# Performance work log

Measured on AMD Instinct MI355X. Metric: run time of the kernel, lower is better.

The kernel has to match this reference:

```python
import jax, jax.numpy as jnp
import numpy as np

B, H, V, T = 32, 1024, 32000, 64

def setup_inputs() -> dict:
    key = jax.random.key(0)
    ks = jax.random.split(key, 8)
    s = 1.0 / np.sqrt(H)
    return {
        "hidden_state": jax.random.normal(ks[0], (1, B, H), jnp.float32),
        "cell_state": jax.random.normal(ks[1], (1, B, H), jnp.float32),
        "W_ih": jax.random.normal(ks[2], (4 * H, H), jnp.float32) * s,
        "W_hh": jax.random.normal(ks[3], (4 * H, H), jnp.float32) * s,
        "b_ih": jax.random.normal(ks[4], (4 * H,), jnp.float32) * s,
        "b_hh": jax.random.normal(ks[5], (4 * H,), jnp.float32) * s,
        "W_out": jax.random.normal(ks[6], (V, H), jnp.float32) * s,
        "b_out": jax.random.normal(ks[7], (V,), jnp.float32) * s,
        "output_len": T,
    }

def reference(hidden_state, cell_state, W_ih, W_hh, b_ih, b_hh, W_out, b_out, output_len):
    h0 = hidden_state[0]  # [B, H]
    c0 = cell_state[0]    # [B, H]
    Hd = h0.shape[-1]
    # Decoder input is all-zeros every step (as in the torch code), so the
    # input-to-hidden contribution reduces to the constant bias b_ih.
    x_gates = jnp.zeros_like(h0) @ W_ih.T + b_ih  # [B, 4H] (keeps W_ih in the graph)

    def step(carry, _):
        h, c = carry
        gates = x_gates + h @ W_hh.T + b_hh  # [B, 4H], torch gate order i,f,g,o
        i, f, g, o = jnp.split(gates, 4, axis=-1)
        c = jax.nn.sigmoid(f) * c + jax.nn.sigmoid(i) * jnp.tanh(g)
        h = jax.nn.sigmoid(o) * jnp.tanh(c)
        logp = jax.nn.log_softmax(h @ W_out.T + b_out, axis=-1)  # [B, V]
        return (h, c), logp

    _, ys = jax.lax.scan(step, (h0, c0), None, length=output_len)  # [T, B, V]
    return jnp.transpose(ys, (1, 0, 2))  # [B, T, V]
```

## Files before the change

kernel.cpp:

```cpp
#include <hip/hip_runtime.h>
#include <hip/hip_bf16.h>
#include <math.h>

#define HD 1024
#define BD 32
#define TD 64
#define VD 32000
#define NWG 128
#define GW  512
#define NTM 16
#define NTN 250

typedef __attribute__((ext_vector_type(8))) short bf16x8;
typedef __attribute__((ext_vector_type(4))) float f32x4;

__device__ __forceinline__ short f2bf(float x) {
    __hip_bfloat16 h = __float2bfloat16(x);
    union { __hip_bfloat16 h; short s; } u; u.h = h; return u.s;
}
__device__ __forceinline__ float fsigmoid(float x) {
    return 1.f / (1.f + __expf(-x));
}
__device__ __forceinline__ float ftanh(float x) {
    return 1.f - 2.f / (__expf(2.f * x) + 1.f);
}


__global__ __launch_bounds__(256) void init_kernel(
    const float* __restrict__ Whh_f, const float* __restrict__ bih,
    const float* __restrict__ bhh,  const float* __restrict__ Wout_f,
    const float* __restrict__ h0,
    short* __restrict__ Whh_b, short* __restrict__ Wout_b,
    float* __restrict__ bias,  short* __restrict__ hb, int* __restrict__ ctr)
{
    long i0 = (long)blockIdx.x * blockDim.x + threadIdx.x;
    long stride = (long)gridDim.x * blockDim.x;
    for (long i = i0; i < 21 * TD; i += stride) ctr[i] = 0;
    for (long i = i0; i < (long)VD * HD / 4; i += stride) {
        float4 x = ((const float4*)Wout_f)[i];
        short4 y; y.x = f2bf(x.x); y.y = f2bf(x.y); y.z = f2bf(x.z); y.w = f2bf(x.w);
        ((short4*)Wout_b)[i] = y;
    }
    for (long i = i0; i < (long)4 * HD * HD / 4; i += stride) {
        float4 x = ((const float4*)Whh_f)[i];
        short4 y; y.x = f2bf(x.x); y.y = f2bf(x.y); y.z = f2bf(x.z); y.w = f2bf(x.w);
        ((short4*)Whh_b)[i] = y;
    }
    for (long i = i0; i < 4 * HD; i += stride) bias[i] = bih[i] + bhh[i];
    for (long i = i0; i < BD * HD; i += stride) {
        int b = (int)(i >> 10), j = (int)(i & 1023);
        int kq = j >> 8, ks = (j >> 5) & 7, hi = (j >> 3) & 3, e = j & 7;
        int u = ((kq * 8 + ks) * 2 + (b >> 4)) * 64 + hi * 16 + (b & 15);
        hb[u * 8 + e] = f2bf(h0[i]);
    }
}

__global__ __launch_bounds__(256, 2) void fused_lstm_gemm(
    const short* __restrict__ Whh_b,
    const float* __restrict__ bias,
    const float* __restrict__ c0,
    short* __restrict__ hb,
    short* __restrict__ Hmat,
    const short* __restrict__ Bw,
    const float* __restrict__ bout,
    float* __restrict__ C,
    int* __restrict__ ctrS,
    int* __restrict__ ctrQ,
    int* __restrict__ queue)
{
    __shared__ alignas(16) char shmem[32768];
    __shared__ int tau_sh;
    const int tid = threadIdx.x;

    if (blockIdx.x < NWG) {
        float (*gl)[32][36] = (float (*)[32][36])shmem;
        const int w = blockIdx.x;
        const int kq = tid >> 6;
        const int l = tid & 63;
        const int lo = l & 15, hi = l >> 4;
        const int j0 = w * 8;
        const int kbase = kq * 256 + hi * 8;

        const short* wB0 = Whh_b + (long)((lo >> 3) * HD + j0 + (lo & 7)) * HD + kbase;
        const short* wB1 = Whh_b + (long)(((16 + lo) >> 3) * HD + j0 + ((16 + lo) & 7)) * HD + kbase;
        bf16x8 wb0[8], wb1[8];
        #pragma unroll
        for (int ks = 0; ks < 8; ks++) {
            wb0[ks] = *(const bf16x8*)(wB0 + ks * 32);
            wb1[ks] = *(const bf16x8*)(wB1 + ks * 32);
        }

        const int cb = tid >> 3, cjl = tid & 7;
        float creg = c0[cb * HD + j0 + cjl];
        const float bi  = bias[j0 + cjl];
        const float bf_ = bias[HD + j0 + cjl];
        const float bg  = bias[2 * HD + j0 + cjl];
        const float bo_ = bias[3 * HD + j0 + cjl];

        const int kq0 = w >> 5, ks0 = (w >> 2) & 7, hi0 = w & 3;
        const int sg = (w >> 3) & 3;
        const int ust = ((kq0 * 8 + ks0) * 2 + (cb >> 4)) * 64 + hi0 * 16 + (cb & 15);

        for (int t = 0; t < TD; ++t) {
            if (t > 0) {
                const int* cq = &ctrQ[kq * TD + (t - 1)];
                while (__hip_atomic_load(cq, __ATOMIC_RELAXED, __HIP_MEMORY_SCOPE_AGENT) < 4)
                    __builtin_amdgcn_s_sleep(1);
            }
            const short* hrb = hb + (size_t)(t & 1) * (BD * HD);

            bf16x8 a0[8], a1[8];
            #pragma unroll
            for (int ks = 0; ks < 8; ks++) {
                const short* p0 = hrb + ((size_t)(((kq * 8 + ks) * 2 + 0) * 64 + l)) * 8;
                const short* p1 = hrb + ((size_t)(((kq * 8 + ks) * 2 + 1) * 64 + l)) * 8;
                asm volatile("global_load_dwordx4 %0, %1, off sc1"
                             : "=v"(a0[ks]) : "v"(p0) : "memory");
                asm volatile("global_load_dwordx4 %0, %1, off sc1"
                             : "=v"(a1[ks]) : "v"(p1) : "memory");
            }
            asm volatile("s_waitcnt vmcnt(0)" ::: "memory");
            __builtin_amdgcn_sched_barrier(0);

            f32x4 acc[2][2] = {};
            #pragma unroll
            for (int ks = 0; ks < 8; ks++) {
                acc[0][0] = __builtin_amdgcn_mfma_f32_16x16x32_bf16(a0[ks], wb0[ks], acc[0][0], 0, 0, 0);
                acc[0][1] = __builtin_amdgcn_mfma_f32_16x16x32_bf16(a0[ks], wb1[ks], acc[0][1], 0, 0, 0);
                acc[1][0] = __builtin_amdgcn_mfma_f32_16x16x32_bf16(a1[ks], wb0[ks], acc[1][0], 0, 0, 0);
                acc[1][1] = __builtin_amdgcn_mfma_f32_16x16x32_bf16(a1[ks], wb1[ks], acc[1][1], 0, 0, 0);
            }
            #pragma unroll
            for (int mf = 0; mf < 2; mf++)
                #pragma unroll
                for (int nf = 0; nf < 2; nf++)
                    #pragma unroll
                    for (int r = 0; r < 4; r++)
                        gl[kq][mf * 16 + hi * 4 + r][nf * 16 + lo] = acc[mf][nf][r];
            __syncthreads();

            float xi = gl[0][cb][cjl]      + gl[1][cb][cjl]      + gl[2][cb][cjl]      + gl[3][cb][cjl]      + bi;
            float xf = gl[0][cb][8 + cjl]  + gl[1][cb][8 + cjl]  + gl[2][cb][8 + cjl]  + gl[3][cb][8 + cjl]  + bf_;
            float xg = gl[0][cb][16 + cjl] + gl[1][cb][16 + cjl] + gl[2][cb][16 + cjl] + gl[3][cb][16 + cjl] + bg;
            float xo = gl[0][cb][24 + cjl] + gl[1][cb][24 + cjl] + gl[2][cb][24 + cjl] + gl[3][cb][24 + cjl] + bo_;
            float cn = fsigmoid(xf) * creg + fsigmoid(xi) * ftanh(xg);
            float hn = fsigmoid(xo) * ftanh(cn);
            creg = cn;
            short hv = f2bf(hn);
            {
                unsigned int hval = (unsigned short)hv;
                short* hm  = Hmat + ((size_t)t * BD + cb) * HD + j0 + cjl;
                short* hwb = hb + (size_t)((t + 1) & 1) * (BD * HD) + (size_t)ust * 8 + cjl;
                asm volatile("global_store_short %0, %1, off sc1" :: "v"(hm),  "v"(hval) : "memory");
                asm volatile("global_store_short %0, %1, off sc1" :: "v"(hwb), "v"(hval) : "memory");
            }
            asm volatile("s_waitcnt vmcnt(0)" ::: "memory");
            __syncthreads();

            if (tid == 0) {
                int old = __hip_atomic_fetch_add(&ctrS[(kq0 * 4 + sg) * TD + t], 1,
                                                 __ATOMIC_RELAXED, __HIP_MEMORY_SCOPE_AGENT);
                if (old == 7)
                    __hip_atomic_fetch_add(&ctrQ[kq0 * TD + t], 1,
                                           __ATOMIC_RELAXED, __HIP_MEMORY_SCOPE_AGENT);
            }
        }
    } else {
        short* lds = (short*)shmem;
        const int lane = tid & 63, wv = tid >> 6;
        const int lo = lane & 15, hi = lane >> 4;
        const int wm = wv >> 1, wn = wv & 1;

        const int u0 = tid, u1 = tid + 256;
        const int r0 = (u0 >> 3) * 2 + (u0 & 1);
        const int r1 = (u1 >> 3) * 2 + (u1 & 1);
        const int kc0 = (((u0 & 7) - (r0 & 7)) & 7) >> 1;
        const int kc1 = (((u1 & 7) - (r1 & 7)) & 7) >> 1;

        int unitA[4], unitB[4];
        #pragma unroll
        for (int mf = 0; mf < 4; mf++) {
            int row = wm * 64 + mf * 16 + lo;
            unitA[mf] = (row >> 1) * 8 + ((2 * hi + (row & 7)) & 7);
        }
        #pragma unroll
        for (int nf = 0; nf < 4; nf++) {
            int row = wn * 64 + nf * 16 + lo;
            unitB[nf] = 512 + (row >> 1) * 8 + ((2 * hi + (row & 7)) & 7);
        }

        for (;;) {
            if (tid == 0)
                tau_sh = __hip_atomic_fetch_add(queue, 1, __ATOMIC_RELAXED, __HIP_MEMORY_SCOPE_AGENT);
            __syncthreads();
            int tau = tau_sh;
            if (tau >= NTM * NTN) break;
            int m = tau / NTN, n = tau - m * NTN;

            if (tid == 0) {
                int tr = m * 4 + 3;
                #pragma unroll
                for (int q = 0; q < 4; q++)
                    while (__hip_atomic_load(&ctrQ[q * TD + tr], __ATOMIC_RELAXED,
                                             __HIP_MEMORY_SCOPE_AGENT) < 4)
                        __builtin_amdgcn_s_sleep(8);
            }
            __syncthreads();

            const short* pA0 = Hmat + ((long)m * 128 + r0) * HD + kc0 * 8;
            const short* pA1 = Hmat + ((long)m * 128 + r1) * HD + kc1 * 8;
            const short* pB0 = Bw + ((long)n * 128 + r0) * HD + kc0 * 8;
            const short* pB1 = Bw + ((long)n * 128 + r1) * HD + kc1 * 8;

#define GSTAGE(koff, bb) do { \
    __builtin_amdgcn_global_load_lds((const __attribute__((address_space(1))) short*)(pA0 + (koff)), \
        (__attribute__((address_space(3))) short*)&lds[((bb) + u0) * 8], 16, 0, 0); \
    __builtin_amdgcn_global_load_lds((const __attribute__((address_space(1))) short*)(pA1 + (koff)), \
        (__attribute__((address_space(3))) short*)&lds[((bb) + u1) * 8], 16, 0, 0); \
    __builtin_amdgcn_global_load_lds((const __attribute__((address_space(1))) short*)(pB0 + (koff)), \
        (__attribute__((address_space(3))) short*)&lds[((bb) + 512 + u0) * 8], 16, 0, 0); \
    __builtin_amdgcn_global_load_lds((const __attribute__((address_space(1))) short*)(pB1 + (koff)), \
        (__attribute__((address_space(3))) short*)&lds[((bb) + 512 + u1) * 8], 16, 0, 0); \
} while (0)

            f32x4 acc[4][4] = {};
            GSTAGE(0, 0);
            GSTAGE(32, 1024);
            asm volatile("s_waitcnt vmcnt(4)\n\ts_barrier" ::: "memory");

            for (int kt = 0; kt < 32; ++kt) {
                const int bb = (kt & 1) * 1024;
                bf16x8 a[4], b[4];
                #pragma unroll
                for (int mf = 0; mf < 4; mf++) a[mf] = *(const bf16x8*)&lds[(bb + unitA[mf]) * 8];
                #pragma unroll
                for (int nf = 0; nf < 4; nf++) b[nf] = *(const bf16x8*)&lds[(bb + unitB[nf]) * 8];
                __builtin_amdgcn_s_setprio(1);
                #pragma unroll
                for (int mf = 0; mf < 4; mf++)
                    #pragma unroll
                    for (int nf = 0; nf < 4; nf++)
                        acc[mf][nf] = __builtin_amdgcn_mfma_f32_16x16x32_bf16(a[mf], b[nf], acc[mf][nf], 0, 0, 0);
                __builtin_amdgcn_s_setprio(0);
                __builtin_amdgcn_s_barrier();
                if (kt + 2 < 32) {
                    GSTAGE((kt + 2) * 32, bb);
                    asm volatile("s_waitcnt vmcnt(4)" ::: "memory");
                } else {
                    asm volatile("s_waitcnt vmcnt(0)" ::: "memory");
                }
                __builtin_amdgcn_s_barrier();
            }
#undef GSTAGE

            float bo[4];
            #pragma unroll
            for (int nf = 0; nf < 4; nf++) bo[nf] = bout[n * 128 + wn * 64 + nf * 16 + lo];
            #pragma unroll
            for (int mf = 0; mf < 4; mf++)
                #pragma unroll
                for (int r = 0; r < 4; r++) {
                    int trow = m * 128 + wm * 64 + mf * 16 + hi * 4 + r;
                    int bt = trow & 31, tt = trow >> 5;
                    float* cp = C + ((long)bt * TD + tt) * VD + n * 128 + wn * 64 + lo;
                    #pragma unroll
                    for (int nf = 0; nf < 4; nf++)
                        cp[nf * 16] = acc[mf][nf][r] + bo[nf];
                }
            __syncthreads();
        }
    }
}

__global__ __launch_bounds__(256) void logsoftmax_inplace(float* __restrict__ C)
{
    const long row = blockIdx.x;
    float* p = C + row * (long)VD;
    const int tid = threadIdx.x;
    float m = -3.4e38f, s = 0.f;
    for (int i = tid; i < VD / 4; i += 256) {
        float4 x = ((const float4*)p)[i];
        float mx = fmaxf(fmaxf(x.x, x.y), fmaxf(x.z, x.w));
        if (mx > m) { s *= __expf(m - mx); m = mx; }
        s += __expf(x.x - m) + __expf(x.y - m) + __expf(x.z - m) + __expf(x.w - m);
    }
    #pragma unroll
    for (int off = 32; off > 0; off >>= 1) {
        float m2 = __shfl_xor(m, off, 64);
        float s2 = __shfl_xor(s, off, 64);
        float mn = fmaxf(m, m2);
        s = s * __expf(m - mn) + s2 * __expf(m2 - mn);
        m = mn;
    }
    __shared__ float sm[4], ss[4];
    if ((tid & 63) == 0) { sm[tid >> 6] = m; ss[tid >> 6] = s; }
    __syncthreads();
    float M = fmaxf(fmaxf(sm[0], sm[1]), fmaxf(sm[2], sm[3]));
    float S = ss[0] * __expf(sm[0] - M) + ss[1] * __expf(sm[1] - M) +
              ss[2] * __expf(sm[2] - M) + ss[3] * __expf(sm[3] - M);
    float lse = M + logf(S);
    for (int i = tid; i < VD / 4; i += 256) {
        float4 x = ((float4*)p)[i];
        x.x -= lse; x.y -= lse; x.z -= lse; x.w -= lse;
        ((float4*)p)[i] = x;
    }
}

extern "C" void kernel_launch(void* const* d_in, const int* in_sizes, int n_in,
                              void* d_out, int out_size, void* d_ws, size_t ws_size,
                              hipStream_t stream)
{
    const float* h0   = (const float*)d_in[0];
    const float* c0   = (const float*)d_in[1];
    const float* Whh  = (const float*)d_in[3];
    const float* bih  = (const float*)d_in[4];
    const float* bhh  = (const float*)d_in[5];
    const float* Wout = (const float*)d_in[6];
    const float* bout = (const float*)d_in[7];

    char* ws = (char*)d_ws;
    short* Wout_b = (short*)ws;  ws += (size_t)VD * HD * 2;
    short* Whh_b  = (short*)ws;  ws += (size_t)4 * HD * HD * 2;
    short* Hmat   = (short*)ws;  ws += (size_t)BD * TD * HD * 2;
    short* hb     = (short*)ws;  ws += (size_t)2 * BD * HD * 2;
    float* bias   = (float*)ws;  ws += (size_t)4 * HD * 4;
    int*   ctr    = (int*)ws;    ws += 21 * TD * sizeof(int);
    float* C      = (float*)d_out;

    int* ctrS  = ctr;
    int* ctrQ  = ctr + 16 * TD;
    int* queue = ctr + 20 * TD;

    init_kernel<<<2048, 256, 0, stream>>>(Whh, bih, bhh, Wout, h0,
                                          Whh_b, Wout_b, bias, hb, ctr);
    fused_lstm_gemm<<<NWG + GW, 256, 0, stream>>>(Whh_b, bias, c0, hb, Hmat,
                                                  Wout_b, bout, C, ctrS, ctrQ, queue);
    logsoftmax_inplace<<<2048, 256, 0, stream>>>(C);
}
```

Before: 502.1 us.

## Fuse softmax row-sum into output GEMM epilogue and enlarge M tile to 256

New measurement: 482.3 us. 3.9% less time.

```diff
diff --git a/kernel.cpp b/kernel.cpp
--- a/kernel.cpp
+++ b/kernel.cpp
@@ -8,8 +8,9 @@
 #define VD 32000
 #define NWG 128
 #define GW  512
-#define NTM 16
+#define NPH 8
 #define NTN 250
+#define NTT (NPH * NTN)
 
 typedef __attribute__((ext_vector_type(8))) short bf16x8;
 typedef __attribute__((ext_vector_type(4))) float f32x4;
@@ -31,11 +32,13 @@
     const float* __restrict__ bhh,  const float* __restrict__ Wout_f,
     const float* __restrict__ h0,
     short* __restrict__ Whh_b, short* __restrict__ Wout_b,
-    float* __restrict__ bias,  short* __restrict__ hb, int* __restrict__ ctr)
+    float* __restrict__ bias,  short* __restrict__ hb, int* __restrict__ ctr,
+    float* __restrict__ rowsum)
 {
     long i0 = (long)blockIdx.x * blockDim.x + threadIdx.x;
     long stride = (long)gridDim.x * blockDim.x;
     for (long i = i0; i < 21 * TD; i += stride) ctr[i] = 0;
+    for (long i = i0; i < BD * TD; i += stride) rowsum[i] = 0.f;
     for (long i = i0; i < (long)VD * HD / 4; i += stride) {
         float4 x = ((const float4*)Wout_f)[i];
         short4 y; y.x = f2bf(x.x); y.y = f2bf(x.y); y.z = f2bf(x.z); y.w = f2bf(x.w);
@@ -64,15 +67,17 @@
     const short* __restrict__ Bw,
     const float* __restrict__ bout,
     float* __restrict__ C,
+    float* __restrict__ rowsum,
     int* __restrict__ ctrS,
     int* __restrict__ ctrQ,
     int* __restrict__ queue)
 {
-    __shared__ alignas(16) char shmem[32768];
+    __shared__ alignas(16) char shmem[50176];
     __shared__ int tau_sh;
     const int tid = threadIdx.x;
 
     if (blockIdx.x < NWG) {
+        __builtin_amdgcn_s_setprio(2);
         float (*gl)[32][36] = (float (*)[32][36])shmem;
         const int w = blockIdx.x;
         const int kq = tid >> 6;
@@ -167,26 +172,35 @@
         }
     } else {
         short* lds = (short*)shmem;
+        float* rowsum_sh = (float*)(shmem + 49152);
         const int lane = tid & 63, wv = tid >> 6;
         const int lo = lane & 15, hi = lane >> 4;
         const int wm = wv >> 1, wn = wv & 1;
 
-        const int u0 = tid, u1 = tid + 256;
-        const int r0 = (u0 >> 3) * 2 + (u0 & 1);
-        const int r1 = (u1 >> 3) * 2 + (u1 & 1);
-        const int kc0 = (((u0 & 7) - (r0 & 7)) & 7) >> 1;
-        const int kc1 = (((u1 & 7) - (r1 & 7)) & 7) >> 1;
-
-        int unitA[4], unitB[4];
-        #pragma unroll
-        for (int mf = 0; mf < 4; mf++) {
-            int row = wm * 64 + mf * 16 + lo;
+        int rA[4], kA[4], rB[2], kB[2];
+        #pragma unroll
+        for (int i = 0; i < 4; i++) {
+            int u = tid + i * 256;
+            rA[i] = (u >> 3) * 2 + (u & 1);
+            kA[i] = (((u & 7) - (rA[i] & 7)) & 7) >> 1;
+        }
+        #pragma unroll
+        for (int i = 0; i < 2; i++) {
+            int u = tid + i * 256;
+            rB[i] = (u >> 3) * 2 + (u & 1);
+            kB[i] = (((u & 7) - (rB[i] & 7)) & 7) >> 1;
+        }
+
+        int unitA[8], unitB[4];
+        #pragma unroll
+        for (int mf = 0; mf < 8; mf++) {
+            int row = wm * 128 + mf * 16 + lo;
             unitA[mf] = (row >> 1) * 8 + ((2 * hi + (row & 7)) & 7);
         }
         #pragma unroll
         for (int nf = 0; nf < 4; nf++) {
-            int row = wn * 64 + nf * 16 + lo;
-            unitB[nf] = 512 + (row >> 1) * 8 + ((2 * hi + (row & 7)) & 7);
+            int brow = wn * 64 + nf * 16 + lo;
+            unitB[nf] = 1024 + (brow >> 1) * 8 + ((2 * hi + (brow & 7)) & 7);
         }
 
         for (;;) {
@@ -194,11 +208,11 @@
                 tau_sh = __hip_atomic_fetch_add(queue, 1, __ATOMIC_RELAXED, __HIP_MEMORY_SCOPE_AGENT);
             __syncthreads();
             int tau = tau_sh;
-            if (tau >= NTM * NTN) break;
-            int m = tau / NTN, n = tau - m * NTN;
+            if (tau >= NTT) break;
+            int p = tau / NTN, n = tau - p * NTN;
 
             if (tid == 0) {
-                int tr = m * 4 + 3;
+                int tr = p * 8 + 7;
                 #pragma unroll
                 for (int q = 0; q < 4; q++)
                     while (__hip_atomic_load(&ctrQ[q * TD + tr], __ATOMIC_RELAXED,
@@ -207,37 +221,43 @@
             }
             __syncthreads();
 
-            const short* pA0 = Hmat + ((long)m * 128 + r0) * HD + kc0 * 8;
-            const short* pA1 = Hmat + ((long)m * 128 + r1) * HD + kc1 * 8;
-            const short* pB0 = Bw + ((long)n * 128 + r0) * HD + kc0 * 8;
-            const short* pB1 = Bw + ((long)n * 128 + r1) * HD + kc1 * 8;
+            const short* pA0 = Hmat + ((long)p * 256 + rA[0]) * HD + kA[0] * 8;
+            const short* pA1 = Hmat + ((long)p * 256 + rA[1]) * HD + kA[1] * 8;
+            const short* pA2 = Hmat + ((long)p * 256 + rA[2]) * HD + kA[2] * 8;
+            const short* pA3 = Hmat + ((long)p * 256 + rA[3]) * HD + kA[3] * 8;
+            const short* pB0 = Bw + ((long)n * 128 + rB[0]) * HD + kB[0] * 8;
+            const short* pB1 = Bw + ((long)n * 128 + rB[1]) * HD + kB[1] * 8;
 
 #define GSTAGE(koff, bb) do { \
     __builtin_amdgcn_global_load_lds((const __attribute__((address_space(1))) short*)(pA0 + (koff)), \
-        (__attribute__((address_space(3))) short*)&lds[((bb) + u0) * 8], 16, 0, 0); \
+        (__attribute__((address_space(3))) short*)&lds[((bb) + tid) * 8], 16, 0, 0); \
     __builtin_amdgcn_global_load_lds((const __attribute__((address_space(1))) short*)(pA1 + (koff)), \
-        (__attribute__((address_space(3))) short*)&lds[((bb) + u1) * 8], 16, 0, 0); \
+        (__attribute__((address_space(3))) short*)&lds[((bb) + tid + 256) * 8], 16, 0, 0); \
+    __builtin_amdgcn_global_load_lds((const __attribute__((address_space(1))) short*)(pA2 + (koff)), \
+        (__attribute__((address_space(3))) short*)&lds[((bb) + tid + 512) * 8], 16, 0, 0); \
+    __builtin_amdgcn_global_load_lds((const __attribute__((address_space(1))) short*)(pA3 + (koff)), \
+        (__attribute__((address_space(3))) short*)&lds[((bb) + tid + 768) * 8], 16, 0, 0); \
     __builtin_amdgcn_global_load_lds((const __attribute__((address_space(1))) short*)(pB0 + (koff)), \
-        (__attribute__((address_space(3))) short*)&lds[((bb) + 512 + u0) * 8], 16, 0, 0); \
+        (__attribute__((address_space(3))) short*)&lds[((bb) + 1024 + tid) * 8], 16, 0, 0); \
     __builtin_amdgcn_global_load_lds((const __attribute__((address_space(1))) short*)(pB1 + (koff)), \
-        (__attribute__((address_space(3))) short*)&lds[((bb) + 512 + u1) * 8], 16, 0, 0); \
+        (__attribute__((address_space(3))) short*)&lds[((bb) + 1024 + tid + 256) * 8], 16, 0, 0); \
 } while (0)
 
-            f32x4 acc[4][4] = {};
+            f32x4 acc[8][4] = {};
             GSTAGE(0, 0);
-            GSTAGE(32, 1024);
-            asm volatile("s_waitcnt vmcnt(4)\n\ts_barrier" ::: "memory");
+            GSTAGE(32, 1536);
+            asm volatile("s_waitcnt vmcnt(6)\n\ts_barrier" ::: "memory");
 
             for (int kt = 0; kt < 32; ++kt) {
-                const int bb = (kt & 1) * 1024;
-                bf16x8 a[4], b[4];
-                #pragma unroll
-                for (int mf = 0; mf < 4; mf++) a[mf] = *(const bf16x8*)&lds[(bb + unitA[mf]) * 8];
+                const int bb = (kt & 1) * 1536;
+                bf16x8 a[8], b[4];
+                #pragma unroll
+                for (int mf = 0; mf < 8; mf++) a[mf] = *(const bf16x8*)&lds[(bb + unitA[mf]) * 8];
                 #pragma unroll
                 for (int nf = 0; nf < 4; nf++) b[nf] = *(const bf16x8*)&lds[(bb + unitB[nf]) * 8];
                 __builtin_amdgcn_s_setprio(1);
                 #pragma unroll
-                for (int mf = 0; mf < 4; mf++)
+                for (int mf = 0; mf < 8; mf++)
                     #pragma unroll
                     for (int nf = 0; nf < 4; nf++)
                         acc[mf][nf] = __builtin_amdgcn_mfma_f32_16x16x32_bf16(a[mf], b[nf], acc[mf][nf], 0, 0, 0);
@@ -245,7 +265,7 @@
                 __builtin_amdgcn_s_barrier();
                 if (kt + 2 < 32) {
                     GSTAGE((kt + 2) * 32, bb);
-                    asm volatile("s_waitcnt vmcnt(4)" ::: "memory");
+                    asm volatile("s_waitcnt vmcnt(6)" ::: "memory");
                 } else {
                     asm volatile("s_waitcnt vmcnt(0)" ::: "memory");
                 }
@@ -253,54 +273,54 @@
             }
 #undef GSTAGE
 
+            rowsum_sh[tid] = 0.f;
+            __syncthreads();
             float bo[4];
             #pragma unroll
             for (int nf = 0; nf < 4; nf++) bo[nf] = bout[n * 128 + wn * 64 + nf * 16 + lo];
             #pragma unroll
-            for (int mf = 0; mf < 4; mf++)
+            for (int mf = 0; mf < 8; mf++)
                 #pragma unroll
                 for (int r = 0; r < 4; r++) {
-                    int trow = m * 128 + wm * 64 + mf * 16 + hi * 4 + r;
+                    int rloc = wm * 128 + mf * 16 + hi * 4 + r;
+                    int trow = p * 256 + rloc;
                     int bt = trow & 31, tt = trow >> 5;
                     float* cp = C + ((long)bt * TD + tt) * VD + n * 128 + wn * 64 + lo;
+                    float es = 0.f;
                     #pragma unroll
-                    for (int nf = 0; nf < 4; nf++)
-                        cp[nf * 16] = acc[mf][nf][r] + bo[nf];
+                    for (int nf = 0; nf < 4; nf++) {
+                        float v = acc[mf][nf][r] + bo[nf];
+                        cp[nf * 16] = v;
+                        es += __expf(v);
+                    }
+                    es += __shfl_xor(es, 1, 64);
+                    es += __shfl_xor(es, 2, 64);
+                    es += __shfl_xor(es, 4, 64);
+                    es += __shfl_xor(es, 8, 64);
+                    if (lo == 0) atomicAdd(&rowsum_sh[rloc], es);
                 }
             __syncthreads();
-        }
-    }
-}
-
-__global__ __launch_bounds__(256) void logsoftmax_inplace(float* __restrict__ C)
+            {
+                int trow = p * 256 + tid;
+                int bt = trow & 31, tt = trow >> 5;
+                float* rp = rowsum + bt * TD + tt;
+                float val = rowsum_sh[tid];
+                asm volatile("global_atomic_add_f32 %0, %1, off" :: "v"(rp), "v"(val) : "memory");
+            }
+            asm volatile("s_waitcnt vmcnt(0)" ::: "memory");
+            __syncthreads();
+        }
+    }
+}
+
+__global__ __launch_bounds__(256) void logsub(float* __restrict__ C,
+                                              const float* __restrict__ rowsum)
 {
     const long row = blockIdx.x;
     float* p = C + row * (long)VD;
-    const int tid = threadIdx.x;
-    float m = -3.4e38f, s = 0.f;
-    for (int i = tid; i < VD / 4; i += 256) {
+    const float lse = logf(rowsum[row]);
+    for (int i = threadIdx.x; i < VD / 4; i += 256) {
         float4 x = ((const float4*)p)[i];
-        float mx = fmaxf(fmaxf(x.x, x.y), fmaxf(x.z, x.w));
-        if (mx > m) { s *= __expf(m - mx); m = mx; }
-        s += __expf(x.x - m) + __expf(x.y - m) + __expf(x.z - m) + __expf(x.w - m);
-    }
-    #pragma unroll
-    for (int off = 32; off > 0; off >>= 1) {
-        float m2 = __shfl_xor(m, off, 64);
-        float s2 = __shfl_xor(s, off, 64);
-        float mn = fmaxf(m, m2);
-        s = s * __expf(m - mn) + s2 * __expf(m2 - mn);
-        m = mn;
-    }
-    __shared__ float sm[4], ss[4];
-    if ((tid & 63) == 0) { sm[tid >> 6] = m; ss[tid >> 6] = s; }
-    __syncthreads();
-    float M = fmaxf(fmaxf(sm[0], sm[1]), fmaxf(sm[2], sm[3]));
-    float S = ss[0] * __expf(sm[0] - M) + ss[1] * __expf(sm[1] - M) +
-              ss[2] * __expf(sm[2] - M) + ss[3] * __expf(sm[3] - M);
-    float lse = M + logf(S);
-    for (int i = tid; i < VD / 4; i += 256) {
-        float4 x = ((float4*)p)[i];
         x.x -= lse; x.y -= lse; x.z -= lse; x.w -= lse;
         ((float4*)p)[i] = x;
     }
@@ -325,6 +345,7 @@
     short* hb     = (short*)ws;  ws += (size_t)2 * BD * HD * 2;
     float* bias   = (float*)ws;  ws += (size_t)4 * HD * 4;
     int*   ctr    = (int*)ws;    ws += 21 * TD * sizeof(int);
+    float* rowsum = (float*)ws;  ws += (size_t)BD * TD * 4;
     float* C      = (float*)d_out;
 
     int* ctrS  = ctr;
@@ -332,8 +353,9 @@
     int* queue = ctr + 20 * TD;
 
     init_kernel<<<2048, 256, 0, stream>>>(Whh, bih, bhh, Wout, h0,
-                                          Whh_b, Wout_b, bias, hb, ctr);
+                                          Whh_b, Wout_b, bias, hb, ctr, rowsum);
     fused_lstm_gemm<<<NWG + GW, 256, 0, stream>>>(Whh_b, bias, c0, hb, Hmat,
-                                                  Wout_b, bout, C, ctrS, ctrQ, queue);
-    logsoftmax_inplace<<<2048, 256, 0, stream>>>(C);
-}
+                                                  Wout_b, bout, C, rowsum,
+                                                  ctrS, ctrQ, queue);
+    logsub<<<2048, 256, 0, stream>>>(C, rowsum);
+}
```

## Fuse softmax exp-sum into GEMM epilogue and use per-block step flags

Applied to the files above, without the earlier changes.

Result: slower. 608.4 us (+21.2%).

```diff
diff --git a/kernel.cpp b/kernel.cpp
--- a/kernel.cpp
+++ b/kernel.cpp
@@ -10,6 +10,7 @@
 #define GW  512
 #define NTM 16
 #define NTN 250
+#define NTT (NTM * NTN)
 
 typedef __attribute__((ext_vector_type(8))) short bf16x8;
 typedef __attribute__((ext_vector_type(4))) float f32x4;
@@ -31,11 +32,13 @@
     const float* __restrict__ bhh,  const float* __restrict__ Wout_f,
     const float* __restrict__ h0,
     short* __restrict__ Whh_b, short* __restrict__ Wout_b,
-    float* __restrict__ bias,  short* __restrict__ hb, int* __restrict__ ctr)
+    float* __restrict__ bias,  short* __restrict__ hb, int* __restrict__ ctr,
+    float* __restrict__ rowsum)
 {
     long i0 = (long)blockIdx.x * blockDim.x + threadIdx.x;
     long stride = (long)gridDim.x * blockDim.x;
-    for (long i = i0; i < 21 * TD; i += stride) ctr[i] = 0;
+    for (long i = i0; i < 256; i += stride) ctr[i] = 0;
+    for (long i = i0; i < BD * TD; i += stride) rowsum[i] = 0.f;
     for (long i = i0; i < (long)VD * HD / 4; i += stride) {
         float4 x = ((const float4*)Wout_f)[i];
         short4 y; y.x = f2bf(x.x); y.y = f2bf(x.y); y.z = f2bf(x.z); y.w = f2bf(x.w);
@@ -64,16 +67,18 @@
     const short* __restrict__ Bw,
     const float* __restrict__ bout,
     float* __restrict__ C,
-    int* __restrict__ ctrS,
-    int* __restrict__ ctrQ,
+    float* __restrict__ rowsum,
+    int* __restrict__ flags,
     int* __restrict__ queue)
 {
-    __shared__ alignas(16) char shmem[32768];
+    __shared__ alignas(16) short lds[2 * 1024 * 8];
+    __shared__ float rowsum_sh[128];
     __shared__ int tau_sh;
     const int tid = threadIdx.x;
 
     if (blockIdx.x < NWG) {
-        float (*gl)[32][36] = (float (*)[32][36])shmem;
+        __builtin_amdgcn_s_setprio(2);
+        float (*gl)[32][36] = (float (*)[32][36])lds;
         const int w = blockIdx.x;
         const int kq = tid >> 6;
         const int l = tid & 63;
@@ -98,14 +103,16 @@
         const float bo_ = bias[3 * HD + j0 + cjl];
 
         const int kq0 = w >> 5, ks0 = (w >> 2) & 7, hi0 = w & 3;
-        const int sg = (w >> 3) & 3;
         const int ust = ((kq0 * 8 + ks0) * 2 + (cb >> 4)) * 64 + hi0 * 16 + (cb & 15);
+        const int* fp = &flags[kq * 32 + (l & 31)];
 
         for (int t = 0; t < TD; ++t) {
             if (t > 0) {
-                const int* cq = &ctrQ[kq * TD + (t - 1)];
-                while (__hip_atomic_load(cq, __ATOMIC_RELAXED, __HIP_MEMORY_SCOPE_AGENT) < 4)
+                for (;;) {
+                    int f = __hip_atomic_load(fp, __ATOMIC_RELAXED, __HIP_MEMORY_SCOPE_AGENT);
+                    if (__all(f >= t)) break;
                     __builtin_amdgcn_s_sleep(1);
+                }
             }
             const short* hrb = hb + (size_t)(t & 1) * (BD * HD);
 
@@ -157,16 +164,10 @@
             asm volatile("s_waitcnt vmcnt(0)" ::: "memory");
             __syncthreads();
 
-            if (tid == 0) {
-                int old = __hip_atomic_fetch_add(&ctrS[(kq0 * 4 + sg) * TD + t], 1,
-                                                 __ATOMIC_RELAXED, __HIP_MEMORY_SCOPE_AGENT);
-                if (old == 7)
-                    __hip_atomic_fetch_add(&ctrQ[kq0 * TD + t], 1,
-                                           __ATOMIC_RELAXED, __HIP_MEMORY_SCOPE_AGENT);
-            }
+            if (tid == 0)
+                __hip_atomic_store(&flags[w], t + 1, __ATOMIC_RELAXED, __HIP_MEMORY_SCOPE_AGENT);
         }
     } else {
-        short* lds = (short*)shmem;
         const int lane = tid & 63, wv = tid >> 6;
         const int lo = lane & 15, hi = lane >> 4;
         const int wm = wv >> 1, wn = wv & 1;
@@ -194,18 +195,23 @@
                 tau_sh = __hip_atomic_fetch_add(queue, 1, __ATOMIC_RELAXED, __HIP_MEMORY_SCOPE_AGENT);
             __syncthreads();
             int tau = tau_sh;
-            if (tau >= NTM * NTN) break;
+            if (tau >= NTT) break;
             int m = tau / NTN, n = tau - m * NTN;
 
-            if (tid == 0) {
-                int tr = m * 4 + 3;
-                #pragma unroll
-                for (int q = 0; q < 4; q++)
-                    while (__hip_atomic_load(&ctrQ[q * TD + tr], __ATOMIC_RELAXED,
-                                             __HIP_MEMORY_SCOPE_AGENT) < 4)
-                        __builtin_amdgcn_s_sleep(8);
-            }
-            __syncthreads();
+            {
+                const int tgt = m * 4 + 4;
+                if (tid < 64) {
+                    const int* f0 = &flags[tid];
+                    const int* f1 = &flags[tid + 64];
+                    for (;;) {
+                        int a = __hip_atomic_load(f0, __ATOMIC_RELAXED, __HIP_MEMORY_SCOPE_AGENT);
+                        int b = __hip_atomic_load(f1, __ATOMIC_RELAXED, __HIP_MEMORY_SCOPE_AGENT);
+                        if (__all(a >= tgt && b >= tgt)) break;
+                        __builtin_amdgcn_s_sleep(16);
+                    }
+                }
+                __syncthreads();
+            }
 
             const short* pA0 = Hmat + ((long)m * 128 + r0) * HD + kc0 * 8;
             const short* pA1 = Hmat + ((long)m * 128 + r1) * HD + kc1 * 8;
@@ -253,6 +259,8 @@
             }
 #undef GSTAGE
 
+            if (tid < 128) rowsum_sh[tid] = 0.f;
+            __syncthreads();
             float bo[4];
             #pragma unroll
             for (int nf = 0; nf < 4; nf++) bo[nf] = bout[n * 128 + wn * 64 + nf * 16 + lo];
@@ -260,47 +268,45 @@
             for (int mf = 0; mf < 4; mf++)
                 #pragma unroll
                 for (int r = 0; r < 4; r++) {
-                    int trow = m * 128 + wm * 64 + mf * 16 + hi * 4 + r;
+                    int rloc = wm * 64 + mf * 16 + hi * 4 + r;
+                    int trow = m * 128 + rloc;
                     int bt = trow & 31, tt = trow >> 5;
                     float* cp = C + ((long)bt * TD + tt) * VD + n * 128 + wn * 64 + lo;
+                    float es = 0.f;
                     #pragma unroll
-                    for (int nf = 0; nf < 4; nf++)
-                        cp[nf * 16] = acc[mf][nf][r] + bo[nf];
+                    for (int nf = 0; nf < 4; nf++) {
+                        float v = acc[mf][nf][r] + bo[nf];
+                        cp[nf * 16] = v;
+                        es += __expf(v);
+                    }
+                    es += __shfl_xor(es, 1, 64);
+                    es += __shfl_xor(es, 2, 64);
+                    es += __shfl_xor(es, 4, 64);
+                    es += __shfl_xor(es, 8, 64);
+                    if (lo == 0) atomicAdd(&rowsum_sh[rloc], es);
                 }
             __syncthreads();
-        }
-    }
-}
-
-__global__ __launch_bounds__(256) void logsoftmax_inplace(float* __restrict__ C)
+            if (tid < 128) {
+                int trow = m * 128 + tid;
+                int bt = trow & 31, tt = trow >> 5;
+                float* rp = rowsum + bt * TD + tt;
+                float val = rowsum_sh[tid];
+                asm volatile("global_atomic_add_f32 %0, %1, off" :: "v"(rp), "v"(val) : "memory");
+            }
+            asm volatile("s_waitcnt vmcnt(0)" ::: "memory");
+            __syncthreads();
+        }
+    }
+}
+
+__global__ __launch_bounds__(256) void logsub(float* __restrict__ C,
+                                              const float* __restrict__ rowsum)
 {
     const long row = blockIdx.x;
     float* p = C + row * (long)VD;
-    const int tid = threadIdx.x;
-    float m = -3.4e38f, s = 0.f;
-    for (int i = tid; i < VD / 4; i += 256) {
+    const float lse = logf(rowsum[row]);
+    for (int i = threadIdx.x; i < VD / 4; i += 256) {
         float4 x = ((const float4*)p)[i];
-        float mx = fmaxf(fmaxf(x.x, x.y), fmaxf(x.z, x.w));
-        if (mx > m) { s *= __expf(m - mx); m = mx; }
-        s += __expf(x.x - m) + __expf(x.y - m) + __expf(x.z - m) + __expf(x.w - m);
-    }
-    #pragma unroll
-    for (int off = 32; off > 0; off >>= 1) {
-        float m2 = __shfl_xor(m, off, 64);
-        float s2 = __shfl_xor(s, off, 64);
-        float mn = fmaxf(m, m2);
-        s = s * __expf(m - mn) + s2 * __expf(m2 - mn);
-        m = mn;
-    }
-    __shared__ float sm[4], ss[4];
-    if ((tid & 63) == 0) { sm[tid >> 6] = m; ss[tid >> 6] = s; }
-    __syncthreads();
-    float M = fmaxf(fmaxf(sm[0], sm[1]), fmaxf(sm[2], sm[3]));
-    float S = ss[0] * __expf(sm[0] - M) + ss[1] * __expf(sm[1] - M) +
-              ss[2] * __expf(sm[2] - M) + ss[3] * __expf(sm[3] - M);
-    float lse = M + logf(S);
-    for (int i = tid; i < VD / 4; i += 256) {
-        float4 x = ((float4*)p)[i];
         x.x -= lse; x.y -= lse; x.z -= lse; x.w -= lse;
         ((float4*)p)[i] = x;
     }
@@ -324,16 +330,17 @@
     short* Hmat   = (short*)ws;  ws += (size_t)BD * TD * HD * 2;
     short* hb     = (short*)ws;  ws += (size_t)2 * BD * HD * 2;
     float* bias   = (float*)ws;  ws += (size_t)4 * HD * 4;
-    int*   ctr    = (int*)ws;    ws += 21 * TD * sizeof(int);
+    int*   ctr    = (int*)ws;    ws += 256 * sizeof(int);
+    float* rowsum = (float*)ws;  ws += (size_t)BD * TD * 4;
     float* C      = (float*)d_out;
 
-    int* ctrS  = ctr;
-    int* ctrQ  = ctr + 16 * TD;
-    int* queue = ctr + 20 * TD;
+    int* flags = ctr;
+    int* queue = ctr + 128;
 
     init_kernel<<<2048, 256, 0, stream>>>(Whh, bih, bhh, Wout, h0,
-                                          Whh_b, Wout_b, bias, hb, ctr);
+                                          Whh_b, Wout_b, bias, hb, ctr, rowsum);
     fused_lstm_gemm<<<NWG + GW, 256, 0, stream>>>(Whh_b, bias, c0, hb, Hmat,
-                                                  Wout_b, bout, C, ctrS, ctrQ, queue);
-    logsoftmax_inplace<<<2048, 256, 0, stream>>>(C);
-}
+                                                  Wout_b, bout, C, rowsum,
+                                                  flags, queue);
+    logsub<<<2048, 256, 0, stream>>>(C, rowsum);
+}
```
